# Performance work log

Hardware: AMD Instinct MI355X
Metric: run time of the kernel (lower is better)

Reference implementation:

```python
import jax, jax.numpy as jnp
import numpy as np

N = 100000      # nodes
E = 1600000     # edges (avg degree 16)
F_DIM = 64      # input feature
H = 64          # hidden1
D1 = 64         # decoder1
P = 200000      # number of query pairs
EPS = 0.0       # GIN eps (train_eps=False)


def setup_inputs() -> dict:
    key = jax.random.key(0)
    ks = jax.random.split(key, 12)
    x = jax.random.normal(ks[0], (N, F_DIM), jnp.float32)
    edge_index = jax.random.randint(ks[1], (2, E), 0, N, dtype=jnp.int32)
    curvature = jax.random.normal(ks[2], (E,), jnp.float32)
    idx = jax.random.randint(ks[3], (2, P), 0, N, dtype=jnp.int32)
    s1 = 1.0 / np.sqrt(F_DIM)
    s2 = 1.0 / np.sqrt(H)
    s3 = 1.0 / np.sqrt(4 * H)
    s4 = 1.0 / np.sqrt(D1)
    w1 = jax.random.uniform(ks[4], (F_DIM, H), jnp.float32, -s1, s1)
    b1 = jax.random.uniform(ks[5], (H,), jnp.float32, -s1, s1)
    w2 = jax.random.uniform(ks[6], (H, H), jnp.float32, -s2, s2)
    b2 = jax.random.uniform(ks[7], (H,), jnp.float32, -s2, s2)
    dw1 = jax.random.uniform(ks[8], (4 * H, D1), jnp.float32, -s3, s3)
    db1 = jax.random.uniform(ks[9], (D1,), jnp.float32, -s3, s3)
    dw2 = jax.random.uniform(ks[10], (D1, 1), jnp.float32, -s4, s4)
    db2 = jax.random.uniform(ks[11], (1,), jnp.float32, -s4, s4)
    return {"x": x, "edge_index": edge_index, "curvature": curvature, "idx": idx,
            "w1": w1, "b1": b1, "w2": w2, "b2": b2,
            "dw1": dw1, "db1": db1, "dw2": dw2, "db2": db2}


def reference(x, edge_index, curvature, idx, w1, b1, w2, b2, dw1, db1, dw2, db2):
    # curvature path: abs + dropout (eval mode => identity), result unused by output
    _ = jnp.abs(curvature)
    src, dst = edge_index[0], edge_index[1]
    # GIN aggregation with self-loops of weight 1: sum_j x_j + x_i
    agg = jax.ops.segment_sum(x[src], dst, num_segments=N) + x  # [N, F]
    h = (1.0 + EPS) * x + agg
    # nn = Linear -> ReLU -> Linear
    h = jnp.maximum(h @ w1 + b1, 0.0) @ w2 + b2                 # [N, H]
    h = jnp.maximum(h, 0.0)                                     # outer ReLU
    e1 = h[idx[0]]                                              # [P, H]
    e2 = h[idx[1]]                                              # [P, H]
    feat = jnp.concatenate([e1 + e2, e1 * e2, e1, e2], axis=1)  # [P, 4H]
    log = jnp.maximum(feat @ dw1 + db1, 0.0) @ dw2 + db2        # [P, 1]
    return log
```

## Files before the change

kernel.cpp:

```cpp
#include <hip/hip_runtime.h>
#include <hip/hip_bf16.h>
#include <hip/hip_fp16.h>
#include <cstdint>

#define N_NODES 100000
#define N_EDGES 1600000
#define FDIM 64
#define NPAIRS 200000
#define NB 391
#define BCAP 4864
#define SSTR 5632
#define EPB 6250

typedef __attribute__((ext_vector_type(8))) _Float16 half8;
typedef __attribute__((ext_vector_type(4))) float floatx4;

__global__ void __launch_bounds__(256) k0_fused(const float4* __restrict__ x4,
        __half* __restrict__ xh, const int* __restrict__ dst,
        int* __restrict__ matrix, int* __restrict__ ovfCnt) {
    __shared__ int hist[NB];
    int blk = blockIdx.x, tid = threadIdx.x;
    int i = blk * 256 + tid;
    if (i == 0) ovfCnt[0] = 0;
    float4 v = x4[i];
    ushort4 o;
    o.x = __half_as_ushort(__float2half(v.x));
    o.y = __half_as_ushort(__float2half(v.y));
    o.z = __half_as_ushort(__float2half(v.z));
    o.w = __half_as_ushort(__float2half(v.w));
    ((ushort4*)xh)[i] = o;
    if (blk < 256) {
        for (int j = tid; j < NB; j += 256) hist[j] = 0;
        __syncthreads();
        int base = blk * EPB;
        for (int j = tid; j < EPB; j += 256)
            atomicAdd(&hist[dst[base + j] >> 8], 1);
        __syncthreads();
        for (int j = tid; j < NB; j += 256) matrix[blk * NB + j] = hist[j];
    }
}

__global__ void __launch_bounds__(256) p1b_scan(int* __restrict__ matrix,
                                                int* __restrict__ bucketCnt) {
    __shared__ int s[256];
    int b = blockIdx.x, t = threadIdx.x;
    int v = matrix[t * NB + b];
    s[t] = v;
    __syncthreads();
    for (int off = 1; off < 256; off <<= 1) {
        int u = (t >= off) ? s[t - off] : 0;
        __syncthreads();
        s[t] += u;
        __syncthreads();
    }
    matrix[t * NB + b] = s[t] - v;
    if (t == 255) bucketCnt[b] = s[255];
}

__global__ void __launch_bounds__(1024) p1c_scatter(const int* __restrict__ src,
        const int* __restrict__ dst, const int* __restrict__ matrix,
        int* __restrict__ bucketArr, int* __restrict__ ovfCnt,
        int2* __restrict__ ovfList) {
    __shared__ int cur[NB];
    int tid = threadIdx.x, blk = blockIdx.x;
    for (int i = tid; i < NB; i += 1024) cur[i] = matrix[blk * NB + i];
    __syncthreads();
    int base = blk * EPB;
    for (int i = tid; i < EPB; i += 1024) {
        int e = base + i;
        int s = src[e], d = dst[e];
        int b = d >> 8;
        int pos = atomicAdd(&cur[b], 1);
        if (pos < BCAP) {
            bucketArr[(size_t)b * SSTR + pos] = ((d & 255) << 17) | s;
        } else {
            int idx = atomicAdd(ovfCnt, 1);
            ovfList[idx] = make_int2(d, s);
        }
    }
}

__global__ void __launch_bounds__(256) p2_build(int* __restrict__ bucketArr,
        const int* __restrict__ bucketCnt, int* __restrict__ rowptr,
        int* __restrict__ deg) {
    __shared__ int ebuf[BCAP];
    __shared__ int hist[256], sc[256], cur[256];
    int b = blockIdx.x, t = threadIdx.x;
    int cnt = bucketCnt[b];
    if (cnt > BCAP) cnt = BCAP;
    int* arr = bucketArr + (size_t)b * SSTR;
    hist[t] = 0;
    __syncthreads();
    for (int i = t; i < cnt; i += 256) {
        int e = arr[i];
        ebuf[i] = e;
        atomicAdd(&hist[(e >> 17) & 255], 1);
    }
    __syncthreads();
    int h = hist[t];
    int pc = (h + 3) & ~3;
    sc[t] = pc;
    __syncthreads();
    for (int off = 1; off < 256; off <<= 1) {
        int u = (t >= off) ? sc[t - off] : 0;
        __syncthreads();
        sc[t] += u;
        __syncthreads();
    }
    int rbase = sc[t] - pc;
    cur[t] = rbase;
    int n = (b << 8) + t;
    if (n < N_NODES) {
        rowptr[n] = b * SSTR + rbase;
        deg[n] = h;
    }
    __syncthreads();
    for (int i = t; i < cnt; i += 256) {
        int e = ebuf[i];
        int dl = (e >> 17) & 255;
        int pos = atomicAdd(&cur[dl], 1);
        arr[pos] = e & 0x1FFFF;
    }
}

__device__ __forceinline__ void addrow(float4& acc, const __half* __restrict__ xh,
                                       int s, int fq) {
    float2 raw = *(const float2*)(xh + (size_t)s * 64 + fq * 4);
    __half2 a = *(__half2*)&raw.x;
    __half2 b = *(__half2*)&raw.y;
    float2 fa = __half22float2(a);
    float2 fb = __half22float2(b);
    acc.x += fa.x; acc.y += fa.y; acc.z += fb.x; acc.w += fb.y;
}

__global__ void __launch_bounds__(256) k2_agg(const __half* __restrict__ xh,
                       __half* __restrict__ h0h, const int* __restrict__ deg,
                       const int* __restrict__ rowptr, const int* __restrict__ csr,
                       const int* __restrict__ ovfCnt,
                       const int2* __restrict__ ovfList,
                       const float* __restrict__ x) {
    int gid = blockIdx.x * 256 + threadIdx.x;
    int n = gid >> 4, fq = gid & 15;
    int dc = deg[n];
    const int4* srow = (const int4*)(csr + rowptr[n]);
    float2 raw = *(const float2*)(xh + (size_t)n * 64 + fq * 4);
    __half2 sa = *(__half2*)&raw.x;
    __half2 sb = *(__half2*)&raw.y;
    float2 fa = __half22float2(sa);
    float2 fb = __half22float2(sb);
    float4 acc = {2.f * fa.x, 2.f * fa.y, 2.f * fb.x, 2.f * fb.y};
    int oc = ovfCnt[0];
    if (oc > 0) {
        for (int i = 0; i < oc; ++i) {
            int2 e = ovfList[i];
            if (e.x == n) {
                const float* xr = x + (size_t)e.y * 64 + fq * 4;
                acc.x += xr[0]; acc.y += xr[1]; acc.z += xr[2]; acc.w += xr[3];
            }
        }
    }
    for (int i = 0; i < dc; i += 16) {
        int4 s4 = srow[i >> 2];
        int4 s5, s6, s7;
        if (i + 4 < dc)  s5 = srow[(i >> 2) + 1];
        if (i + 8 < dc)  s6 = srow[(i >> 2) + 2];
        if (i + 12 < dc) s7 = srow[(i >> 2) + 3];
        addrow(acc, xh, s4.x, fq);
        if (i + 1 < dc)  addrow(acc, xh, s4.y, fq);
        if (i + 2 < dc)  addrow(acc, xh, s4.z, fq);
        if (i + 3 < dc)  addrow(acc, xh, s4.w, fq);
        if (i + 4 < dc)  addrow(acc, xh, s5.x, fq);
        if (i + 5 < dc)  addrow(acc, xh, s5.y, fq);
        if (i + 6 < dc)  addrow(acc, xh, s5.z, fq);
        if (i + 7 < dc)  addrow(acc, xh, s5.w, fq);
        if (i + 8 < dc)  addrow(acc, xh, s6.x, fq);
        if (i + 9 < dc)  addrow(acc, xh, s6.y, fq);
        if (i + 10 < dc) addrow(acc, xh, s6.z, fq);
        if (i + 11 < dc) addrow(acc, xh, s6.w, fq);
        if (i + 12 < dc) addrow(acc, xh, s7.x, fq);
        if (i + 13 < dc) addrow(acc, xh, s7.y, fq);
        if (i + 14 < dc) addrow(acc, xh, s7.z, fq);
        if (i + 15 < dc) addrow(acc, xh, s7.w, fq);
    }
    ushort4 st;
    st.x = __half_as_ushort(__float2half(acc.x));
    st.y = __half_as_ushort(__float2half(acc.y));
    st.z = __half_as_ushort(__float2half(acc.z));
    st.w = __half_as_ushort(__float2half(acc.w));
    ((ushort4*)h0h)[(size_t)n * 16 + fq] = st;
}

__global__ void __launch_bounds__(256) k3_mfma(const __half* __restrict__ h,
        __half* __restrict__ hh, const float* __restrict__ w1,
        const float* __restrict__ b1, const float* __restrict__ w2,
        const float* __restrict__ b2) {
    __shared__ half8 WF1[512], WF2[512];
    __shared__ float Tbuf[4 * 16 * 68];
    int tid = threadIdx.x;
    for (int f = tid; f < 512; f += 256) {
        int lane = f & 63, st = f >> 6;
        int t = st & 3, kh = st >> 2;
        int q = lane >> 4, nl = lane & 15;
        int n = t * 16 + nl;
        int K0 = kh * 32 + q * 8;
        half8 hv1, hv2;
#pragma unroll
        for (int j = 0; j < 8; ++j) {
            hv1[j] = (_Float16)w1[(K0 + j) * 64 + n];
            hv2[j] = (_Float16)w2[(K0 + j) * 64 + n];
        }
        WF1[f] = hv1;
        WF2[f] = hv2;
    }
    __syncthreads();
    int lane = tid & 63;
    int q = lane >> 4, p = lane & 15;
    int wtid0 = blockIdx.x * 4 + (tid >> 6);
    int wtid = wtid0 < 6249 ? wtid0 : 6249;
    int n0 = wtid * 16;
    float b1t[4], b2t[4];
#pragma unroll
    for (int t = 0; t < 4; ++t) {
        b1t[t] = b1[t * 16 + p];
        b2t[t] = b2[t * 16 + p];
    }
    const half8* hrow = (const half8*)(h + (size_t)(n0 + p) * 64);
    half8 A0 = hrow[q], A1 = hrow[4 + q];
    floatx4 acc[4];
#pragma unroll
    for (int t = 0; t < 4; ++t) acc[t] = (floatx4){0.f, 0.f, 0.f, 0.f};
#pragma unroll
    for (int t = 0; t < 4; ++t) {
        acc[t] = __builtin_amdgcn_mfma_f32_16x16x32_f16(A0, WF1[t * 64 + lane],
                                                        acc[t], 0, 0, 0);
        acc[t] = __builtin_amdgcn_mfma_f32_16x16x32_f16(A1, WF1[(4 + t) * 64 + lane],
                                                        acc[t], 0, 0, 0);
    }
    float* T = Tbuf + (tid >> 6) * (16 * 68);
#pragma unroll
    for (int t = 0; t < 4; ++t) {
#pragma unroll
        for (int r = 0; r < 4; ++r)
            T[(q * 4 + r) * 68 + t * 16 + p] = fmaxf(acc[t][r] + b1t[t], 0.f);
    }
    const float* Tp = T + p * 68;
    float4 u0 = *(const float4*)(Tp + q * 8);
    float4 u1 = *(const float4*)(Tp + q * 8 + 4);
    float4 u2 = *(const float4*)(Tp + 32 + q * 8);
    float4 u3 = *(const float4*)(Tp + 32 + q * 8 + 4);
    half8 g0, g1;
    g0[0] = (_Float16)u0.x; g0[1] = (_Float16)u0.y;
    g0[2] = (_Float16)u0.z; g0[3] = (_Float16)u0.w;
    g0[4] = (_Float16)u1.x; g0[5] = (_Float16)u1.y;
    g0[6] = (_Float16)u1.z; g0[7] = (_Float16)u1.w;
    g1[0] = (_Float16)u2.x; g1[1] = (_Float16)u2.y;
    g1[2] = (_Float16)u2.z; g1[3] = (_Float16)u2.w;
    g1[4] = (_Float16)u3.x; g1[5] = (_Float16)u3.y;
    g1[6] = (_Float16)u3.z; g1[7] = (_Float16)u3.w;
#pragma unroll
    for (int t = 0; t < 4; ++t) acc[t] = (floatx4){0.f, 0.f, 0.f, 0.f};
#pragma unroll
    for (int t = 0; t < 4; ++t) {
        acc[t] = __builtin_amdgcn_mfma_f32_16x16x32_f16(g0, WF2[t * 64 + lane],
                                                        acc[t], 0, 0, 0);
        acc[t] = __builtin_amdgcn_mfma_f32_16x16x32_f16(g1, WF2[(4 + t) * 64 + lane],
                                                        acc[t], 0, 0, 0);
    }
    if (wtid0 < 6250) {
#pragma unroll
        for (int t = 0; t < 4; ++t) {
#pragma unroll
            for (int r = 0; r < 4; ++r)
                hh[(size_t)(n0 + q * 4 + r) * 64 + t * 16 + p] =
                    __float2half(fmaxf(acc[t][r] + b2t[t], 0.f));
        }
    }
}

__global__ void __launch_bounds__(512) k4_pair(const __half* __restrict__ hh,
                        const int* __restrict__ qidx,
                        const float* __restrict__ dw1, const float* __restrict__ db1,
                        const float* __restrict__ dw2, const float* __restrict__ db2,
                        float* __restrict__ out, int numWaves) {
    __shared__ half8 BF[1536];
    int tid = threadIdx.x;
    for (int f = tid; f < 1536; f += 512) {
        int lane = f & 63, st = f >> 6;
        int t = st & 3, s = st >> 2;
        int sec = s >> 1, kh = s & 1;
        int q = lane >> 4, nl = lane & 15;
        int n = t * 16 + nl;
        int K0 = kh * 32 + q * 8;
        half8 hv;
#pragma unroll
        for (int j = 0; j < 8; ++j) {
            int k = K0 + j;
            float v;
            if (sec == 0)      v = dw1[k * 64 + n] + dw1[(128 + k) * 64 + n];
            else if (sec == 1) v = dw1[k * 64 + n] + dw1[(192 + k) * 64 + n];
            else               v = dw1[(64 + k) * 64 + n];
            hv[j] = (_Float16)v;
        }
        BF[f] = hv;
    }
    __syncthreads();
    int lane = tid & 63;
    int q = lane >> 4, nl = lane & 15;
    float db1t[4], dw2t[4];
#pragma unroll
    for (int t = 0; t < 4; ++t) {
        db1t[t] = db1[t * 16 + nl];
        dw2t[t] = dw2[t * 16 + nl];
    }
    float db2v = db2[0];
    int wid = (blockIdx.x * 512 + tid) >> 6;
    for (int task = wid; task < NPAIRS / 16; task += numWaves) {
        int p0 = task * 16;
        int i1 = qidx[p0 + nl];
        int i2 = qidx[NPAIRS + p0 + nl];
        const half8* r1 = (const half8*)(hh + (size_t)i1 * 64);
        const half8* r2 = (const half8*)(hh + (size_t)i2 * 64);
        half8 e1a = r1[q],     e1b = r1[4 + q];
        half8 e2a = r2[q],     e2b = r2[4 + q];
        half8 pA = e1a * e2a,  pB = e1b * e2b;
        floatx4 acc[4];
#pragma unroll
        for (int t = 0; t < 4; ++t) acc[t] = (floatx4){0.f, 0.f, 0.f, 0.f};

#define DO_STEP(S, AV)                                                        \
        _Pragma("unroll")                                                     \
        for (int t = 0; t < 4; ++t)                                           \
            acc[t] = __builtin_amdgcn_mfma_f32_16x16x32_f16(                  \
                (AV), BF[((S) * 4 + t) * 64 + lane], acc[t], 0, 0, 0);

        DO_STEP(0, e1a)
        DO_STEP(1, e1b)
        DO_STEP(2, e2a)
        DO_STEP(3, e2b)
        DO_STEP(4, pA)
        DO_STEP(5, pB)
#undef DO_STEP

        float part[4] = {0.f, 0.f, 0.f, 0.f};
#pragma unroll
        for (int t = 0; t < 4; ++t) {
#pragma unroll
            for (int r = 0; r < 4; ++r)
                part[r] = fmaf(fmaxf(acc[t][r] + db1t[t], 0.f), dw2t[t], part[r]);
        }
#pragma unroll
        for (int off = 1; off < 16; off <<= 1) {
#pragma unroll
            for (int r = 0; r < 4; ++r) part[r] += __shfl_xor(part[r], off, 64);
        }
        if (nl == 0) {
#pragma unroll
            for (int r = 0; r < 4; ++r) out[p0 + q * 4 + r] = part[r] + db2v;
        }
    }
}

extern "C" void kernel_launch(void* const* d_in, const int* in_sizes, int n_in,
                              void* d_out, int out_size, void* d_ws, size_t ws_size,
                              hipStream_t stream) {
    const float* x    = (const float*)d_in[0];
    const int*   eidx = (const int*)d_in[1];
    const int*   qidx = (const int*)d_in[3];
    const float* w1   = (const float*)d_in[4];
    const float* b1   = (const float*)d_in[5];
    const float* w2   = (const float*)d_in[6];
    const float* b2   = (const float*)d_in[7];
    const float* dw1  = (const float*)d_in[8];
    const float* db1  = (const float*)d_in[9];
    const float* dw2  = (const float*)d_in[10];
    const float* db2  = (const float*)d_in[11];
    float* out = (float*)d_out;

    char* ws = (char*)d_ws;
    __half* h0h       = (__half*)ws;
    __half* xh        = (__half*)(ws + 12800000);
    int*    bucketArr = (int*)(ws + 25600000);
    int2*   ovfList   = (int2*)(ws + 34408448);
    int*    rowptr    = (int*)(ws + 47208448);
    int*    deg       = (int*)(ws + 47608448);
    int*    matrix    = (int*)(ws + 48008448);
    int*    bucketCnt = (int*)(ws + 48408832);
    int*    ovfCnt    = (int*)(ws + 48410396);

    const int* src = eidx;
    const int* dst = eidx + N_EDGES;

    k0_fused<<<6250, 256, 0, stream>>>((const float4*)x, xh, dst, matrix, ovfCnt);
    p1b_scan<<<NB, 256, 0, stream>>>(matrix, bucketCnt);
    p1c_scatter<<<256, 1024, 0, stream>>>(src, dst, matrix, bucketArr,
                                          ovfCnt, ovfList);
    p2_build<<<NB, 256, 0, stream>>>(bucketArr, bucketCnt, rowptr, deg);
    k2_agg<<<6250, 256, 0, stream>>>(xh, h0h, deg, rowptr, bucketArr,
                                     ovfCnt, ovfList, x);
    k3_mfma<<<1563, 256, 0, stream>>>(h0h, xh, w1, b1, w2, b2);
    k4_pair<<<782, 512, 0, stream>>>(xh, qidx, dw1, db1, dw2, db2, out, 6256);
}
```

Baseline: 225.7 us.

## Sort neighbor lists by source window and widen aggregation to 4 threads per node

The build kernel now insertion-sorts each node's neighbor list by source id and records per-window neighbor counts (windows of 16384 source nodes) packed into a uint2. The aggregation kernel uses 4 threads per node with 16 features each, using two 16-byte loads per neighbor row instead of one 8-byte load. It walks neighbors window by window, intended to improve L2 locality of the gathered rows across the grid. The per-thread serial insertion sort adds work to p2_build, and the wider per-thread accumulator raises register use.

```diff
diff --git a/kernel.cpp b/kernel.cpp
--- a/kernel.cpp
+++ b/kernel.cpp
@@ -11,8 +11,11 @@
 #define BCAP 4864
 #define SSTR 5632
 #define EPB 6250
+#define WINSHIFT 14
+#define NWIN 7
 
 typedef __attribute__((ext_vector_type(8))) _Float16 half8;
+typedef __attribute__((ext_vector_type(8))) unsigned short ushort8;
 typedef __attribute__((ext_vector_type(4))) float floatx4;
 
 __global__ void __launch_bounds__(256) k0_fused(const float4* __restrict__ x4,
@@ -82,7 +85,7 @@
 
 __global__ void __launch_bounds__(256) p2_build(int* __restrict__ bucketArr,
         const int* __restrict__ bucketCnt, int* __restrict__ rowptr,
-        int* __restrict__ deg) {
+        int* __restrict__ deg, uint2* __restrict__ wdeg) {
     __shared__ int ebuf[BCAP];
     __shared__ int hist[256], sc[256], cur[256];
     int b = blockIdx.x, t = threadIdx.x;
@@ -121,73 +124,117 @@
         int pos = atomicAdd(&cur[dl], 1);
         arr[pos] = e & 0x1FFFF;
     }
-}
-
-__device__ __forceinline__ void addrow(float4& acc, const __half* __restrict__ xh,
-                                       int s, int fq) {
-    float2 raw = *(const float2*)(xh + (size_t)s * 64 + fq * 4);
-    __half2 a = *(__half2*)&raw.x;
-    __half2 b = *(__half2*)&raw.y;
-    float2 fa = __half22float2(a);
-    float2 fb = __half22float2(b);
-    acc.x += fa.x; acc.y += fa.y; acc.z += fb.x; acc.w += fb.y;
-}
-
-__global__ void __launch_bounds__(256) k2_agg(const __half* __restrict__ xh,
+    __syncthreads();
+    for (int i = 1; i < h; ++i) {
+        int v = arr[rbase + i];
+        int j = i - 1;
+        while (j >= 0 && arr[rbase + j] > v) {
+            arr[rbase + j + 1] = arr[rbase + j];
+            --j;
+        }
+        arr[rbase + j + 1] = v;
+    }
+    unsigned wlo = 0, whi = 0;
+    for (int i = 0; i < h; ++i) {
+        int wv = arr[rbase + i] >> WINSHIFT;
+        if (wv < 4) wlo += 1u << (8 * wv);
+        else        whi += 1u << (8 * (wv - 4));
+    }
+    if (n < N_NODES) {
+        uint2 wd; wd.x = wlo; wd.y = whi;
+        wdeg[n] = wd;
+    }
+}
+
+__device__ __forceinline__ void addrow32(float* acc,
+        const __half* __restrict__ xh, int s, int fq) {
+    const __half* p = xh + (size_t)s * 64 + fq * 16;
+    float4 r0 = *(const float4*)p;
+    float4 r1 = *(const float4*)(p + 8);
+    const __half2* h0 = (const __half2*)&r0;
+    const __half2* h1 = (const __half2*)&r1;
+#pragma unroll
+    for (int j = 0; j < 4; ++j) {
+        float2 f = __half22float2(h0[j]);
+        acc[2 * j]     += f.x;
+        acc[2 * j + 1] += f.y;
+    }
+#pragma unroll
+    for (int j = 0; j < 4; ++j) {
+        float2 f = __half22float2(h1[j]);
+        acc[8 + 2 * j]     += f.x;
+        acc[8 + 2 * j + 1] += f.y;
+    }
+}
+
+__global__ void __launch_bounds__(256, 8) k2_agg(const __half* __restrict__ xh,
                        __half* __restrict__ h0h, const int* __restrict__ deg,
                        const int* __restrict__ rowptr, const int* __restrict__ csr,
+                       const uint2* __restrict__ wdeg,
                        const int* __restrict__ ovfCnt,
                        const int2* __restrict__ ovfList,
                        const float* __restrict__ x) {
-    int gid = blockIdx.x * 256 + threadIdx.x;
-    int n = gid >> 4, fq = gid & 15;
-    int dc = deg[n];
-    const int4* srow = (const int4*)(csr + rowptr[n]);
-    float2 raw = *(const float2*)(xh + (size_t)n * 64 + fq * 4);
-    __half2 sa = *(__half2*)&raw.x;
-    __half2 sb = *(__half2*)&raw.y;
-    float2 fa = __half22float2(sa);
-    float2 fb = __half22float2(sb);
-    float4 acc = {2.f * fa.x, 2.f * fa.y, 2.f * fb.x, 2.f * fb.y};
+    int unit = blockIdx.x * 256 + threadIdx.x;
+    if (unit >= N_NODES * 4) return;
+    int n = unit >> 2, fq = unit & 3;
+    const __half* selfp = xh + (size_t)n * 64 + fq * 16;
+    float4 r0 = *(const float4*)selfp;
+    float4 r1 = *(const float4*)(selfp + 8);
+    float acc[16];
+    {
+        const __half2* h0 = (const __half2*)&r0;
+        const __half2* h1 = (const __half2*)&r1;
+#pragma unroll
+        for (int j = 0; j < 4; ++j) {
+            float2 f = __half22float2(h0[j]);
+            acc[2 * j]     = 2.f * f.x;
+            acc[2 * j + 1] = 2.f * f.y;
+        }
+#pragma unroll
+        for (int j = 0; j < 4; ++j) {
+            float2 f = __half22float2(h1[j]);
+            acc[8 + 2 * j]     = 2.f * f.x;
+            acc[8 + 2 * j + 1] = 2.f * f.y;
+        }
+    }
     int oc = ovfCnt[0];
     if (oc > 0) {
         for (int i = 0; i < oc; ++i) {
             int2 e = ovfList[i];
             if (e.x == n) {
-                const float* xr = x + (size_t)e.y * 64 + fq * 4;
-                acc.x += xr[0]; acc.y += xr[1]; acc.z += xr[2]; acc.w += xr[3];
+                const float* xr = x + (size_t)e.y * 64 + fq * 16;
+#pragma unroll
+                for (int j = 0; j < 16; ++j) acc[j] += xr[j];
             }
         }
     }
-    for (int i = 0; i < dc; i += 16) {
-        int4 s4 = srow[i >> 2];
-        int4 s5, s6, s7;
-        if (i + 4 < dc)  s5 = srow[(i >> 2) + 1];
-        if (i + 8 < dc)  s6 = srow[(i >> 2) + 2];
-        if (i + 12 < dc) s7 = srow[(i >> 2) + 3];
-        addrow(acc, xh, s4.x, fq);
-        if (i + 1 < dc)  addrow(acc, xh, s4.y, fq);
-        if (i + 2 < dc)  addrow(acc, xh, s4.z, fq);
-        if (i + 3 < dc)  addrow(acc, xh, s4.w, fq);
-        if (i + 4 < dc)  addrow(acc, xh, s5.x, fq);
-        if (i + 5 < dc)  addrow(acc, xh, s5.y, fq);
-        if (i + 6 < dc)  addrow(acc, xh, s5.z, fq);
-        if (i + 7 < dc)  addrow(acc, xh, s5.w, fq);
-        if (i + 8 < dc)  addrow(acc, xh, s6.x, fq);
-        if (i + 9 < dc)  addrow(acc, xh, s6.y, fq);
-        if (i + 10 < dc) addrow(acc, xh, s6.z, fq);
-        if (i + 11 < dc) addrow(acc, xh, s6.w, fq);
-        if (i + 12 < dc) addrow(acc, xh, s7.x, fq);
-        if (i + 13 < dc) addrow(acc, xh, s7.y, fq);
-        if (i + 14 < dc) addrow(acc, xh, s7.z, fq);
-        if (i + 15 < dc) addrow(acc, xh, s7.w, fq);
-    }
-    ushort4 st;
-    st.x = __half_as_ushort(__float2half(acc.x));
-    st.y = __half_as_ushort(__float2half(acc.y));
-    st.z = __half_as_ushort(__float2half(acc.z));
-    st.w = __half_as_ushort(__float2half(acc.w));
-    ((ushort4*)h0h)[(size_t)n * 16 + fq] = st;
+    const int* row = csr + rowptr[n];
+    uint2 wd = wdeg[n];
+    int c = 0;
+#pragma unroll
+    for (int w = 0; w < NWIN; ++w) {
+        int cnt = ((w < 4) ? (wd.x >> (8 * w)) : (wd.y >> (8 * (w - 4)))) & 255;
+        for (int i = 0; i < cnt; i += 4) {
+            int rem = cnt - i;
+            int s0 = row[c];
+            int s1 = row[c + 1];
+            int s2 = row[c + 2];
+            int s3 = row[c + 3];
+            addrow32(acc, xh, s0, fq);
+            if (rem > 1) addrow32(acc, xh, s1, fq);
+            if (rem > 2) addrow32(acc, xh, s2, fq);
+            if (rem > 3) addrow32(acc, xh, s3, fq);
+            c += (rem < 4) ? rem : 4;
+        }
+    }
+    ushort8 lo, hi;
+#pragma unroll
+    for (int j = 0; j < 8; ++j) lo[j] = __half_as_ushort(__float2half(acc[j]));
+#pragma unroll
+    for (int j = 0; j < 8; ++j) hi[j] = __half_as_ushort(__float2half(acc[8 + j]));
+    __half* op = h0h + (size_t)n * 64 + fq * 16;
+    *(ushort8*)op = lo;
+    *(ushort8*)(op + 8) = hi;
 }
 
 __global__ void __launch_bounds__(256) k3_mfma(const __half* __restrict__ h,
@@ -381,6 +428,7 @@
     __half* xh        = (__half*)(ws + 12800000);
     int*    bucketArr = (int*)(ws + 25600000);
     int2*   ovfList   = (int2*)(ws + 34408448);
+    uint2*  wdeg      = (uint2*)(ws + 42408448);
     int*    rowptr    = (int*)(ws + 47208448);
     int*    deg       = (int*)(ws + 47608448);
     int*    matrix    = (int*)(ws + 48008448);
@@ -394,8 +442,8 @@
     p1b_scan<<<NB, 256, 0, stream>>>(matrix, bucketCnt);
     p1c_scatter<<<256, 1024, 0, stream>>>(src, dst, matrix, bucketArr,
                                           ovfCnt, ovfList);
-    p2_build<<<NB, 256, 0, stream>>>(bucketArr, bucketCnt, rowptr, deg);
-    k2_agg<<<6250, 256, 0, stream>>>(xh, h0h, deg, rowptr, bucketArr,
+    p2_build<<<NB, 256, 0, stream>>>(bucketArr, bucketCnt, rowptr, deg, wdeg);
+    k2_agg<<<1563, 256, 0, stream>>>(xh, h0h, deg, rowptr, bucketArr, wdeg,
                                      ovfCnt, ovfList, x);
     k3_mfma<<<1563, 256, 0, stream>>>(h0h, xh, w1, b1, w2, b2);
     k4_pair<<<782, 512, 0, stream>>>(xh, qidx, dw1, db1, dw2, db2, out, 6256);
```

Result: slower. 323.7 us (+43.4%).
